# Optimization experiments

Measured on AMD Instinct MI355X. Metric: run time of the kernel, lower is better.

Reference implementation:

```python
import jax, jax.numpy as jnp
import numpy as np

B, L = 64, 200
NQ = 1024          # n_question == output_dim
NPID = 4096
D = 256            # q_embed_dim
H = 512            # hidden_dim
Q = 1024           # output_dim
L2 = 1e-05


def setup_inputs() -> dict:
    key = jax.random.key(0)
    ks = jax.random.split(key, 20)
    q_data = jax.random.randint(ks[0], (B, L), 1, NQ + 1)          # question ids in [1, NQ]
    ans = jax.random.randint(ks[1], (B, L), 0, 2)
    qa_data = q_data + NQ * ans                                     # encoded (q, answer)
    pid_data = jax.random.randint(ks[2], (B, L), 0, NPID + 1)
    matrix = jax.random.uniform(ks[3], (Q, Q), jnp.float32) * 0.05  # p_c_relations
    u = jax.random.uniform(ks[4], (B, L))
    target = jnp.where(u < 0.1, -1.0, jnp.where(u < 0.55, 0.0, 1.0)).astype(jnp.float32)
    s = 0.05
    q_emb = jax.random.normal(ks[5], (NQ + 1, D), jnp.float32) * s
    qa_emb = jax.random.normal(ks[6], (2, D), jnp.float32) * s
    q_emb_diff = jax.random.normal(ks[7], (NQ + 1, D), jnp.float32) * s
    qa_emb_diff = jax.random.normal(ks[8], (2 * NQ + 1, D), jnp.float32) * s
    diff_parm = jax.random.normal(ks[9], (NPID + 1, 1), jnp.float32) * s
    gs = 1.0 / np.sqrt(H).astype(np.float32)
    w_ih = jax.random.uniform(ks[10], (3 * H, 2 * D), jnp.float32, -gs, gs)
    w_hh = jax.random.uniform(ks[11], (3 * H, H), jnp.float32, -gs, gs)
    b_ih = jax.random.uniform(ks[12], (3 * H,), jnp.float32, -gs, gs)
    b_hh = jax.random.uniform(ks[13], (3 * H,), jnp.float32, -gs, gs)
    fc_w = jax.random.normal(ks[14], (Q, H), jnp.float32) * 0.02
    fc_b = jnp.zeros((Q,), jnp.float32)
    return dict(q_data=q_data, qa_data=qa_data, pid_data=pid_data, matrix=matrix,
                target=target, q_emb=q_emb, qa_emb=qa_emb, q_emb_diff=q_emb_diff,
                qa_emb_diff=qa_emb_diff, diff_parm=diff_parm, w_ih=w_ih, w_hh=w_hh,
                b_ih=b_ih, b_hh=b_hh, fc_w=fc_w, fc_b=fc_b)


def _gru(x, w_ih, w_hh, b_ih, b_hh):
    # PyTorch GRU, single layer, batch_first. x: [B, L, In]
    xg = jnp.einsum('bli,gi->blg', x, w_ih) + b_ih          # [B, L, 3H]
    def step(h, xg_t):
        hg = h @ w_hh.T + b_hh
        xr, xz, xn = jnp.split(xg_t, 3, axis=-1)
        hr, hz, hn = jnp.split(hg, 3, axis=-1)
        r = jax.nn.sigmoid(xr + hr)
        z = jax.nn.sigmoid(xz + hz)
        n = jnp.tanh(xn + r * hn)
        h_new = (1.0 - z) * n + z * h
        return h_new, h_new
    h0 = jnp.zeros((x.shape[0], w_hh.shape[1]), x.dtype)
    _, hs = jax.lax.scan(step, h0, xg.transpose(1, 0, 2))
    return hs.transpose(1, 0, 2)                             # [B, L, H]


def reference(q_data, qa_data, pid_data, matrix, target, q_emb, qa_emb,
              q_emb_diff, qa_emb_diff, diff_parm, w_ih, w_hh, b_ih, b_hh,
              fc_w, fc_b):
    q_embed = q_emb[q_data]                                  # [B, L, D]
    qa = (qa_data - q_data) // NQ                            # answer in {0,1}
    qa_embed = qa_emb[qa] + q_embed
    pid_embed = diff_parm[pid_data]                          # [B, L, 1]
    q_embed2 = q_embed + pid_embed * q_emb_diff[q_data]
    qa_embed2 = qa_embed + pid_embed * qa_emb_diff[qa]
    c_reg = (pid_embed ** 2).sum() * L2

    x = jnp.concatenate([qa_embed2, q_embed2], axis=-1)      # [B, L, 2D]
    gru_out = _gru(x, w_ih, w_hh, b_ih, b_hh)
    gru_out = jnp.einsum('blh,qh->blq', gru_out, fc_w) + fc_b  # [B, L, Q]

    got = jnp.einsum('blq,kq->blk', gru_out, matrix)         # [B, L, Q]
    master = jnp.where(got >= 0.4, 1.0, got)                 # threshold-to-1 only
    # mastery of the question asked at step t: master[b, t, q-1]
    mvals = jnp.take_along_axis(master, (q_data - 1)[..., None], axis=2)[..., 0]  # [B, L]

    f32 = jnp.float32
    eq = (q_data[:, :, None] == q_data[:, None, :]).astype(f32)   # [B, t, k]
    t_idx = jnp.arange(L)
    tri_strict = (t_idx[:, None] > t_idx[None, :]).astype(f32)    # k < t
    tri_incl = (t_idx[:, None] >= t_idx[None, :]).astype(f32)     # k <= t
    mast = (mvals == 1.0).astype(f32)
    notm = (mvals == 0.0).astype(f32)
    qa1 = (qa == 1).astype(f32)
    qa0 = 1.0 - qa1
    base = eq * tri_strict                                        # [B, L, L]
    mc = jnp.einsum('btk,bk->bt', base, qa1 * mast)   # master_correct
    mi = jnp.einsum('btk,bk->bt', base, qa0 * mast)   # master_incorrect
    nmc = jnp.einsum('btk,bk->bt', base, qa0 * notm)  # no_master_correct
    aa = jnp.einsum('btk,tk->bt', eq, tri_incl)       # answered_all (>= 1)

    arB = jnp.arange(B)
    idx = q_data - 1

    def dina_step(carry, xs):
        guess, slip = carry                            # [B, Q] each
        i_t, m_t, qa_t, mc_t, mi_t, nmc_t, aa_t = xs   # [B] each
        g_upd = jnp.where(m_t == 1.0, mc_t / aa_t,
                          jnp.where(qa_t == 0, 1.0 - nmc_t / aa_t, nmc_t / aa_t))
        upd_slip = (m_t == 1.0) & (qa_t == 0)
        new_g = jnp.where(upd_slip, guess[arB, i_t], g_upd)
        new_s = jnp.where(upd_slip, mi_t / aa_t, slip[arB, i_t])
        guess = guess.at[arB, i_t].set(new_g)
        slip = slip.at[arB, i_t].set(new_s)
        p = (1.0 - new_s) * (m_t * new_g + (1.0 - new_s) * (1.0 - m_t))
        return (guess, slip), p

    init = (jnp.zeros((B, Q), f32), jnp.zeros((B, Q), f32))
    xs = (idx.T, mvals.T, qa.T, mc.T, mi.T, nmc.T, aa.T)
    _, ps = jax.lax.scan(dina_step, init, xs)          # [L, B]
    preds = ps.T.reshape(-1)                           # [B*L]

    labels = target.reshape(-1)
    mask = labels > -0.9
    preds_d = jax.lax.stop_gradient(preds)             # torch detaches via torch.tensor()
    mse_sum = (((preds_d - labels) ** 2) * mask.astype(f32)).sum()
    loss = mse_sum + c_reg
    return (loss, jax.nn.sigmoid(preds_d), mask.sum())
```

## Files before the change

kernel.cpp:

```cpp
#include <hip/hip_runtime.h>
#include <hip/hip_bf16.h>
#include <math.h>

#define BB 64
#define LL 200
#define NQ 1024
#define DD 256
#define HH 512
#define QQ 1024
#define G3 1536
#define BL 12800
#define GBLK 256

#define OFF_ACC   ((size_t)0)
#define OFF_CELLS ((size_t)16)
#define OFF_HA    ((size_t)1056)
#define OFF_AQ    (OFF_HA + 65536)
#define OFF_DQ    (OFF_AQ + 1574400)
#define OFF_BQA   (OFF_DQ + 1574400)
#define OFF_CQA   (OFF_BQA + 3072)
#define OFF_WSUM  (OFF_CQA + 3072)
#define OFF_FCWT  (OFF_WSUM + 393216)
#define OFF_M2    (OFF_FCWT + 524288)
#define OFF_MB    (OFF_M2 + 524288)
#define OFF_QINT  (OFF_MB + 1024)
#define OFF_QAINT (OFF_QINT + 12800)
#define OFF_PIDF  (OFF_QAINT + 12800)

typedef float f32x4 __attribute__((ext_vector_type(4)));

__device__ __forceinline__ float wave_sum64(float v) {
    #pragma unroll
    for (int o = 32; o > 0; o >>= 1) v += __shfl_down(v, o, 64);
    return v;
}

__device__ __forceinline__ f32x4 llc_load4(const float* p) {
    f32x4 v;
    asm volatile("global_load_dwordx4 %0, %1, off sc0 sc1" : "=v"(v) : "v"(p));
    return v;
}
__device__ __forceinline__ void llc_wait2(f32x4& a, f32x4& b) {
    asm volatile("s_waitcnt vmcnt(0)" : "+v"(a), "+v"(b));
}
__device__ __forceinline__ void llc_store1(float* p, float v) {
    asm volatile("global_store_dword %0, %1, off sc0 sc1" :: "v"(p), "v"(v) : "memory");
}

__device__ __forceinline__ float quad_sum(float v) {
    float t1 = __int_as_float(__builtin_amdgcn_update_dpp(
        0, __float_as_int(v), 0xB1, 0xF, 0xF, true));
    v += t1;
    float t2 = __int_as_float(__builtin_amdgcn_update_dpp(
        0, __float_as_int(v), 0x4E, 0xF, 0xF, true));
    return v + t2;
}

__device__ __forceinline__ void gemm_nt_body(
    const float* __restrict__ A, int lda, const float* __restrict__ B, int ldb,
    float* __restrict__ C, int ldc, int M, int N, int K,
    const float* __restrict__ bias, int bm, int bn, int tid, bool sumB,
    float (*As)[129], float (*Bs)[65])
{
    const int tx = tid & 15, ty = tid >> 4;
    const int mm = tid >> 4, kk = tid & 15;
    float acc[8][4] = {};
    float ar[8], br[4];
    #pragma unroll
    for (int i = 0; i < 8; ++i) {
        int m = bm + mm + 16 * i;
        ar[i] = (m < M) ? A[(size_t)m * lda + kk] : 0.f;
    }
    #pragma unroll
    for (int i = 0; i < 4; ++i) {
        int n = bn + mm + 16 * i;
        br[i] = (n < N) ? (sumB ? (B[(size_t)n * ldb + kk] + B[(size_t)n * ldb + DD + kk])
                                : B[(size_t)n * ldb + kk]) : 0.f;
    }
    for (int k0 = 0; k0 < K; k0 += 16) {
        #pragma unroll
        for (int i = 0; i < 8; ++i) As[kk][mm + 16 * i] = ar[i];
        #pragma unroll
        for (int i = 0; i < 4; ++i) Bs[kk][mm + 16 * i] = br[i];
        __syncthreads();
        int kn = k0 + 16;
        if (kn < K) {
            #pragma unroll
            for (int i = 0; i < 8; ++i) {
                int m = bm + mm + 16 * i;
                ar[i] = (m < M) ? A[(size_t)m * lda + kn + kk] : 0.f;
            }
            #pragma unroll
            for (int i = 0; i < 4; ++i) {
                int n = bn + mm + 16 * i;
                br[i] = (n < N) ? (sumB ? (B[(size_t)n * ldb + kn + kk]
                                           + B[(size_t)n * ldb + DD + kn + kk])
                                        : B[(size_t)n * ldb + kn + kk]) : 0.f;
            }
        }
        #pragma unroll
        for (int kq = 0; kq < 16; ++kq) {
            float a[8], b[4];
            #pragma unroll
            for (int i = 0; i < 8; ++i) a[i] = As[kq][ty * 8 + i];
            #pragma unroll
            for (int j = 0; j < 4; ++j) b[j] = Bs[kq][tx * 4 + j];
            #pragma unroll
            for (int i = 0; i < 8; ++i)
                #pragma unroll
                for (int j = 0; j < 4; ++j) acc[i][j] += a[i] * b[j];
        }
        __syncthreads();
    }
    #pragma unroll
    for (int i = 0; i < 8; ++i) {
        int m = bm + ty * 8 + i;
        if (m >= M) continue;
        #pragma unroll
        for (int j = 0; j < 4; ++j) {
            int n = bn + tx * 4 + j;
            if (n >= N) continue;
            C[(size_t)m * ldc + n] = acc[i][j] + (bias ? bias[n] : 0.f);
        }
    }
}

__global__ __launch_bounds__(256) void prep_all(
    const float* __restrict__ q_emb, const float* __restrict__ q_emb_diff,
    const float* __restrict__ qa_emb, const float* __restrict__ qa_emb_diff,
    const float* __restrict__ w_ih, const float* __restrict__ b_ih,
    float* __restrict__ Aq, float* __restrict__ Dq,
    float* __restrict__ Bqa, float* __restrict__ Cqa,
    const float* __restrict__ matrix, const float* __restrict__ fc_w,
    const float* __restrict__ fc_b, float* __restrict__ M2, float* __restrict__ mb,
    const int* __restrict__ q_data, const int* __restrict__ qa_data,
    const int* __restrict__ pid_data, const float* __restrict__ diff_parm,
    int* __restrict__ qint, int* __restrict__ qaint, float* __restrict__ pidf,
    float* __restrict__ acc_g, float* __restrict__ hA)
{
    __shared__ float As[16][129];
    __shared__ float Bs[16][65];
    __shared__ float sm[4];
    const int tid = threadIdx.x;
    const int widx = blockIdx.x;

    if (widx < 128) {
        const int bm = (widx >> 3) * 64, bn = (widx & 7) * 64;
        const int kk = tid & 15, mm = tid >> 4;
        const int nb = tid & 63, kb2 = tid >> 6;
        const int tx = tid & 15, ty = tid >> 4;
        float acc[4][4] = {};
        for (int k0 = 0; k0 < QQ; k0 += 16) {
            if (k0) __syncthreads();
            #pragma unroll
            for (int i = 0; i < 4; ++i)
                As[kk][mm + 16 * i] = matrix[(size_t)(bm + mm + 16 * i) * QQ + k0 + kk];
            #pragma unroll
            for (int i = 0; i < 4; ++i)
                Bs[kb2 + 4 * i][nb] = fc_w[(size_t)(k0 + kb2 + 4 * i) * HH + bn + nb];
            __syncthreads();
            #pragma unroll
            for (int kq = 0; kq < 16; ++kq) {
                float a[4], b[4];
                #pragma unroll
                for (int i = 0; i < 4; ++i) a[i] = As[kq][ty * 4 + i];
                #pragma unroll
                for (int j = 0; j < 4; ++j) b[j] = Bs[kq][tx * 4 + j];
                #pragma unroll
                for (int i = 0; i < 4; ++i)
                    #pragma unroll
                    for (int j = 0; j < 4; ++j) acc[i][j] += a[i] * b[j];
            }
        }
        #pragma unroll
        for (int i = 0; i < 4; ++i)
            #pragma unroll
            for (int j = 0; j < 4; ++j)
                M2[(size_t)(bm + ty * 4 + i) * HH + bn + tx * 4 + j] = acc[i][j];
        return;
    }
    if (widx < 560) {
        const int w2 = widx - 128;
        const int z = w2 >= 216;
        const int w3 = z ? w2 - 216 : w2;
        const int bm = (w3 / 24) * 128, bn = (w3 % 24) * 64;
        gemm_nt_body(z ? q_emb_diff : q_emb, DD,
                     z ? (w_ih + DD) : w_ih, 2 * DD,
                     z ? Dq : Aq, G3, NQ + 1, G3, DD,
                     nullptr, bm, bn, tid, !z, As, Bs);
        return;
    }
    if (widx < 608) {
        const int w2 = widx - 560;
        const int z = w2 >= 24;
        const int bn = (z ? w2 - 24 : w2) * 64;
        gemm_nt_body(z ? qa_emb_diff : qa_emb, DD,
                     w_ih, 2 * DD,
                     z ? Cqa : Bqa, G3, 2, G3, DD,
                     z ? nullptr : b_ih, 0, bn, tid, false, As, Bs);
        return;
    }
    if (widx < 612) {
        const int wv2 = tid >> 6, lane2 = tid & 63;
        const int kb = (widx - 608) * 256 + wv2 * 64;
        for (int i = 0; i < 64; ++i) {
            const float* mrow = matrix + (size_t)(kb + i) * QQ;
            float sacc = 0.f;
            #pragma unroll
            for (int j = 0; j < 16; ++j)
                sacc += mrow[lane2 + 64 * j] * fc_b[lane2 + 64 * j];
            sacc = wave_sum64(sacc);
            if (lane2 == 0) mb[kb + i] = sacc;
        }
        return;
    }
    if (widx < 662) {
        int r = (widx - 612) * 256 + tid;
        float pp = 0.f;
        if (r < BL) {
            int q = q_data[r];
            qint[r] = q;
            qaint[r] = (qa_data[r] - q) / NQ;
            float pid = diff_parm[pid_data[r]];
            pidf[r] = pid;
            pp = pid * pid;
        }
        pp = wave_sum64(pp);
        int lane = tid & 63, w = tid >> 6;
        if (lane == 0) sm[w] = pp;
        __syncthreads();
        if (tid == 0) atomicAdd(&acc_g[0], sm[0] + sm[1] + sm[2] + sm[3]);
        return;
    }
    {
        float* dst = hA + (size_t)(widx - 662) * 4096 + tid;
        #pragma unroll
        for (int i = 0; i < 16; ++i) dst[i * 256] = 0.f;
    }
}

__global__ __launch_bounds__(512) void gru_persist(
    const float* __restrict__ Aq,
    const float* __restrict__ Dq,
    const float* __restrict__ Bqa,
    const float* __restrict__ Cqa,
    const int* __restrict__ qint,
    const int* __restrict__ qaint,
    const float* __restrict__ pidf,
    const float* __restrict__ w_hh,
    const float* __restrict__ b_hh,
    float* __restrict__ hA,
    const float* __restrict__ M2,
    const float* __restrict__ mbv,
    unsigned int* __restrict__ cells,
    const float* __restrict__ target,
    float* __restrict__ out,
    float* __restrict__ acc_g)
{
    __shared__ float hs[8][512];
    __shared__ float part[8][3][16][8];
    __shared__ float bqs[2][3][16];
    __shared__ float cqs[2][3][16];
    __shared__ int smq[8][200];
    __shared__ int smqa[8][200];
    __shared__ float smp[8][200];
    __shared__ float mvbuf[LL];

    const int tid = threadIdx.x;
    const int bid = blockIdx.x;
    const int bg = bid >> 5;
    const int ug = bid & 31;
    const int j0 = ug * 16;
    const int wv = tid >> 6;
    const int lane = tid & 63;
    const int g = lane >> 2;
    const int s = lane & 3;

    if (tid < 96) {
        const int qa = tid / 48, rem = tid - qa * 48;
        const int gate = rem >> 4, u = rem & 15;
        bqs[qa][gate][u] = Bqa[(size_t)qa * G3 + gate * HH + j0 + u];
        cqs[qa][gate][u] = Cqa[(size_t)qa * G3 + gate * HH + j0 + u];
    }
    for (int i = tid; i < 8 * LL; i += 512) {
        const int c = i / LL, tt = i - c * LL;
        const int col = bg * 8 + c;
        smq[c][tt] = qint[col * LL + tt];
        smqa[c][tt] = qaint[col * LL + tt];
        smp[c][tt] = pidf[col * LL + tt];
    }

    f32x4 ws4[3][4];
    #pragma unroll
    for (int gate = 0; gate < 3; ++gate)
        #pragma unroll
        for (int q = 0; q < 4; ++q)
            ws4[gate][q] = *(const f32x4*)&w_hh[
                (size_t)(gate * HH + j0 + g) * HH + wv * 64 + q * 16 + s * 4];

    const int eu = tid >> 3;
    const int eb = tid & 7;
    float bhr = 0.f, bhz = 0.f, bhn = 0.f;
    if (tid < 128) {
        bhr = b_hh[j0 + eu];
        bhz = b_hh[HH + j0 + eu];
        bhn = b_hh[2 * HH + j0 + eu];
    }

    const int b0 = lane >> 4;
    const int c0 = (lane & 15) * 4;

    __syncthreads();

    for (int t = 0; t < LL; ++t) {
        float xr = 0.f, xz = 0.f, xn = 0.f;
        if (tid < 128) {
            const int q = smq[eb][t];
            const int qa = smqa[eb][t];
            const float pid = smp[eb][t];
            const float* aq = Aq + (size_t)q * G3 + j0 + eu;
            const float* dq = Dq + (size_t)q * G3 + j0 + eu;
            float ar_ = aq[0], az_ = aq[HH], an_ = aq[2 * HH];
            float dr_ = dq[0], dz_ = dq[HH], dn_ = dq[2 * HH];
            xr = ar_ + bqs[qa][0][eu] + pid * (cqs[qa][0][eu] + dr_);
            xz = az_ + bqs[qa][1][eu] + pid * (cqs[qa][1][eu] + dz_);
            xn = an_ + bqs[qa][2][eu] + pid * (cqs[qa][2][eu] + dn_);
        }
        f32x4 m2a = {0.f, 0.f, 0.f, 0.f}, m2b = {0.f, 0.f, 0.f, 0.f};
        float mbq = 0.f;
        if (wv == 2 && ug < 8 && t >= 1) {
            const int q = smq[ug][t - 1] - 1;
            const float* m2r = M2 + (size_t)q * HH + lane * 8;
            m2a = *(const f32x4*)m2r;
            m2b = *(const f32x4*)(m2r + 4);
            mbq = mbv[q];
        }
        if (t && tid < 64) {
            const unsigned want = (unsigned)t;
            for (;;) {
                unsigned v = want;
                if (lane < 32)
                    v = __hip_atomic_load(&cells[(bg * 32 + lane) * 4],
                                          __ATOMIC_RELAXED, __HIP_MEMORY_SCOPE_AGENT);
                if (__all((int)(v >= want))) break;
                __builtin_amdgcn_s_sleep(2);
            }
        }
        __syncthreads();

        {
            const float* hcur = hA + (size_t)(t & 1) * (HH * BB);
            const float* p0 = hcur + (size_t)(bg * 8 + b0) * HH + wv * 64 + c0;
            f32x4 va = llc_load4(p0);
            f32x4 vb = llc_load4(p0 + 4 * HH);
            llc_wait2(va, vb);
            *(f32x4*)&hs[wv][b0 * 64 + ((c0 + 8 * b0) & 63)] = va;
            *(f32x4*)&hs[wv][(b0 + 4) * 64 + ((c0 + 8 * b0 + 32) & 63)] = vb;
        }

        float acc[3][8];
        #pragma unroll
        for (int gate = 0; gate < 3; ++gate) {
            #pragma unroll
            for (int b = 0; b < 8; ++b) acc[gate][b] = 0.f;
        }
        #pragma unroll
        for (int q = 0; q < 4; ++q) {
            const int cb = q * 16 + s * 4;
            #pragma unroll
            for (int b = 0; b < 8; ++b) {
                f32x4 h4 = *(const f32x4*)&hs[wv][b * 64 + ((cb + 8 * b) & 63)];
                #pragma unroll
                for (int gate = 0; gate < 3; ++gate) {
                    acc[gate][b] += ws4[gate][q].x * h4.x + ws4[gate][q].y * h4.y
                                  + ws4[gate][q].z * h4.z + ws4[gate][q].w * h4.w;
                }
            }
        }

        #pragma unroll
        for (int gate = 0; gate < 3; ++gate)
            #pragma unroll
            for (int b = 0; b < 8; ++b)
                acc[gate][b] = quad_sum(acc[gate][b]);

        if (s < 3) {
            const int rot = (2 * ((g >> 2) + s)) & 7;
            #pragma unroll
            for (int hp = 0; hp < 4; ++hp) {
                const int b = hp * 2;
                float e0 = (s == 0) ? acc[0][b]     : (s == 1) ? acc[1][b]     : acc[2][b];
                float e1 = (s == 0) ? acc[0][b + 1] : (s == 1) ? acc[1][b + 1] : acc[2][b + 1];
                const int bp = (b + rot) & 7;
                *(float2*)&part[wv][s][g][bp] = make_float2(e0, e1);
            }
        }
        __syncthreads();

        if (wv == 2 && ug < 8 && t >= 1) {
            float sacc = 0.f;
            #pragma unroll
            for (int j = 0; j < 8; ++j) {
                const int k = lane * 8 + j;
                const float hv = hs[k >> 6][ug * 64 + (((k & 63) + 8 * ug) & 63)];
                const float mvw = (j == 0) ? m2a.x : (j == 1) ? m2a.y : (j == 2) ? m2a.z
                                : (j == 3) ? m2a.w : (j == 4) ? m2b.x : (j == 5) ? m2b.y
                                : (j == 6) ? m2b.z : m2b.w;
                sacc += hv * mvw;
            }
            sacc = wave_sum64(sacc);
            if (lane == 0) {
                float sv = sacc + mbq;
                mvbuf[t - 1] = (sv >= 0.4f) ? 1.0f : sv;
            }
        }

        if (tid < 128) {
            const int rb = eu >> 2;
            const int bp0 = (eb + 2 * (rb + 0)) & 7;
            const int bp1 = (eb + 2 * (rb + 1)) & 7;
            const int bp2 = (eb + 2 * (rb + 2)) & 7;
            float sg0 = 0.f, sg1 = 0.f, sg2 = 0.f;
            #pragma unroll
            for (int w = 0; w < 8; ++w) {
                sg0 += part[w][0][eu][bp0];
                sg1 += part[w][1][eu][bp1];
                sg2 += part[w][2][eu][bp2];
            }
            const int ku = j0 + eu;
            float hprev = hs[ku >> 6][eb * 64 + (((ku & 63) + 8 * eb) & 63)];
            float rg = 1.f / (1.f + expf(-(xr + sg0 + bhr)));
            float zg = 1.f / (1.f + expf(-(xz + sg1 + bhz)));
            float ng = tanhf(xn + rg * (sg2 + bhn));
            float hn = (1.f - zg) * ng + zg * hprev;
            llc_store1(hA + (size_t)((t + 1) & 1) * (HH * BB)
                          + (size_t)(bg * 8 + eb) * HH + ku, hn);
            asm volatile("s_waitcnt vmcnt(0)" ::: "memory");
        }
        __syncthreads();
        if (tid == 0)
            __hip_atomic_store(&cells[bid * 4], (unsigned)(t + 1),
                               __ATOMIC_RELAXED, __HIP_MEMORY_SCOPE_AGENT);
    }

    if (ug >= 8) return;
    if (tid < 64) {
        const unsigned want = (unsigned)LL;
        for (;;) {
            unsigned v = want;
            if (lane < 32)
                v = __hip_atomic_load(&cells[(bg * 32 + lane) * 4],
                                      __ATOMIC_RELAXED, __HIP_MEMORY_SCOPE_AGENT);
            if (__all((int)(v >= want))) break;
            __builtin_amdgcn_s_sleep(2);
        }
    }
    __syncthreads();
    {
        const float* hcur = hA + (size_t)(LL & 1) * (HH * BB);
        const float* p0 = hcur + (size_t)(bg * 8 + b0) * HH + wv * 64 + c0;
        f32x4 va = llc_load4(p0);
        f32x4 vb = llc_load4(p0 + 4 * HH);
        llc_wait2(va, vb);
        *(f32x4*)&hs[wv][b0 * 64 + ((c0 + 8 * b0) & 63)] = va;
        *(f32x4*)&hs[wv][(b0 + 4) * 64 + ((c0 + 8 * b0 + 32) & 63)] = vb;
    }
    __syncthreads();
    if (wv == 2) {
        const int q = smq[ug][LL - 1] - 1;
        const float* m2r = M2 + (size_t)q * HH + lane * 8;
        f32x4 ma = *(const f32x4*)m2r;
        f32x4 mc4 = *(const f32x4*)(m2r + 4);
        float sacc = 0.f;
        #pragma unroll
        for (int j = 0; j < 8; ++j) {
            const int k = lane * 8 + j;
            const float hv = hs[k >> 6][ug * 64 + (((k & 63) + 8 * ug) & 63)];
            const float mvw = (j == 0) ? ma.x : (j == 1) ? ma.y : (j == 2) ? ma.z
                            : (j == 3) ? ma.w : (j == 4) ? mc4.x : (j == 5) ? mc4.y
                            : (j == 6) ? mc4.z : mc4.w;
            sacc += hv * mvw;
        }
        sacc = wave_sum64(sacc);
        if (lane == 0) {
            float sv = sacc + mbv[q];
            mvbuf[LL - 1] = (sv >= 0.4f) ? 1.0f : sv;
        }
    }
    __syncthreads();

    const int bq = bg * 8 + ug;
    float* guess = &hs[0][0];
    float* slip = &hs[2][0];
    float* preds_l = &hs[4][0];
    float* s_mc = &part[0][0][0][0];
    float* s_mi = s_mc + 256;
    float* s_nmc = s_mc + 512;
    float* s_aa = s_mc + 768;
    float* sred = &bqs[0][0][0];
    float* cred = sred + 8;
    for (int i = tid; i < QQ; i += 512) { guess[i] = 0.f; slip[i] = 0.f; }
    if (tid < LL) {
        const int qt = smq[ug][tid];
        float smc = 0.f, smi = 0.f, snmc = 0.f, saa = 0.f;
        for (int k = 0; k <= tid; ++k) {
            if (smq[ug][k] == qt) {
                saa += 1.f;
                if (k < tid) {
                    float mk = (mvbuf[k] == 1.f) ? 1.f : 0.f;
                    float nk = (mvbuf[k] == 0.f) ? 1.f : 0.f;
                    float a1 = (smqa[ug][k] == 1) ? 1.f : 0.f;
                    smc += a1 * mk;
                    smi += (1.f - a1) * mk;
                    snmc += (1.f - a1) * nk;
                }
            }
        }
        s_mc[tid] = smc;
        s_mi[tid] = smi;
        s_nmc[tid] = snmc;
        s_aa[tid] = saa;
    }
    __syncthreads();
    if (tid == 0) {
        for (int t = 0; t < LL; ++t) {
            const int i = smq[ug][t] - 1;
            const float m = mvbuf[t];
            const int qa = smqa[ug][t];
            const float aat = s_aa[t];
            float g_upd = (m == 1.f) ? s_mc[t] / aat
                          : ((qa == 0) ? 1.f - s_nmc[t] / aat : s_nmc[t] / aat);
            bool us = (m == 1.f) && (qa == 0);
            float ng = us ? guess[i] : g_upd;
            float ns = us ? s_mi[t] / aat : slip[i];
            guess[i] = ng;
            slip[i] = ns;
            preds_l[t] = (1.f - ns) * (m * ng + (1.f - ns) * (1.f - m));
        }
    }
    __syncthreads();
    if (tid < 256) {
        float lm = 0.f, lc = 0.f;
        if (tid < LL) {
            const float p = preds_l[tid];
            const float lab = target[bq * LL + tid];
            const float msk = (lab > -0.9f) ? 1.f : 0.f;
            const float d = p - lab;
            lm = d * d * msk;
            lc = msk;
            out[1 + bq * LL + tid] = 1.f / (1.f + expf(-p));
        }
        lm = wave_sum64(lm);
        lc = wave_sum64(lc);
        if (lane == 0) { sred[wv] = lm; cred[wv] = lc; }
    }
    __syncthreads();
    if (tid == 0) {
        atomicAdd(&acc_g[1], sred[0] + sred[1] + sred[2] + sred[3]);
        atomicAdd(&acc_g[2], cred[0] + cred[1] + cred[2] + cred[3]);
        const unsigned old = __hip_atomic_fetch_add(&cells[1021], 1u,
                                                    __ATOMIC_ACQ_REL,
                                                    __HIP_MEMORY_SCOPE_AGENT);
        if (old == 63) {
            float a0 = __hip_atomic_load(&acc_g[0], __ATOMIC_RELAXED, __HIP_MEMORY_SCOPE_AGENT);
            float a1 = __hip_atomic_load(&acc_g[1], __ATOMIC_RELAXED, __HIP_MEMORY_SCOPE_AGENT);
            float a2 = __hip_atomic_load(&acc_g[2], __ATOMIC_RELAXED, __HIP_MEMORY_SCOPE_AGENT);
            out[0] = a1 + a0 * 1e-5f;
            out[1 + BL] = a2;
        }
    }
}

extern "C" void kernel_launch(void* const* d_in, const int* in_sizes, int n_in,
                              void* d_out, int out_size, void* d_ws, size_t ws_size,
                              hipStream_t stream) {
    const int* q_data = (const int*)d_in[0];
    const int* qa_data = (const int*)d_in[1];
    const int* pid_data = (const int*)d_in[2];
    const float* matrix = (const float*)d_in[3];
    const float* target = (const float*)d_in[4];
    const float* q_emb = (const float*)d_in[5];
    const float* qa_emb = (const float*)d_in[6];
    const float* q_emb_diff = (const float*)d_in[7];
    const float* qa_emb_diff = (const float*)d_in[8];
    const float* diff_parm = (const float*)d_in[9];
    const float* w_ih = (const float*)d_in[10];
    const float* w_hh = (const float*)d_in[11];
    const float* b_ih = (const float*)d_in[12];
    const float* b_hh = (const float*)d_in[13];
    const float* fc_w = (const float*)d_in[14];
    const float* fc_b = (const float*)d_in[15];
    float* out = (float*)d_out;
    float* W = (float*)d_ws;

    float* acc = W + OFF_ACC;
    unsigned int* cells = (unsigned int*)(W + OFF_CELLS);
    float* hA = W + OFF_HA;
    float* Aq = W + OFF_AQ;
    float* Dq = W + OFF_DQ;
    float* Bqa = W + OFF_BQA;
    float* Cqa = W + OFF_CQA;
    float* M2 = W + OFF_M2;
    float* mb = W + OFF_MB;
    int* qint = (int*)(W + OFF_QINT);
    int* qaint = (int*)(W + OFF_QAINT);
    float* pidf = W + OFF_PIDF;

    hipMemsetAsync(W, 0, 1056 * sizeof(float), stream);

    prep_all<<<678, 256, 0, stream>>>(
        q_emb, q_emb_diff, qa_emb, qa_emb_diff, w_ih, b_ih,
        Aq, Dq, Bqa, Cqa, matrix, fc_w, fc_b, M2, mb,
        q_data, qa_data, pid_data, diff_parm, qint, qaint, pidf, acc, hA);

    gru_persist<<<GBLK, 512, 0, stream>>>(Aq, Dq, Bqa, Cqa, qint, qaint, pidf,
                                          w_hh, b_hh, hA, M2, mb, cells,
                                          target, out, acc);
}
```

Measured before the change: 1.005 ms.

## Parallelize DINA scan per timestep, fold memset into prep, drop per-step barrier

The serial single-thread DINA recurrence over 200 steps is replaced by per-timestep threads that scan backwards for the last guess/slip update of the same question, turning a sequential loop into parallel lookback. The hipMemsetAsync of the counter/accumulator region is folded into an extra prep_all block, and the pid-regularizer atomics become per-block partial stores summed at the end. In the GRU step loop every thread now spins on the cell flags itself and the following __syncthreads is removed, which cuts a barrier but raises polling traffic and risks hs buffer reuse hazards.

```diff
diff --git a/kernel.cpp b/kernel.cpp
--- a/kernel.cpp
+++ b/kernel.cpp
@@ -19,8 +19,8 @@
 #define OFF_DQ    (OFF_AQ + 1574400)
 #define OFF_BQA   (OFF_DQ + 1574400)
 #define OFF_CQA   (OFF_BQA + 3072)
-#define OFF_WSUM  (OFF_CQA + 3072)
-#define OFF_FCWT  (OFF_WSUM + 393216)
+#define OFF_CREGS (OFF_CQA + 3072)
+#define OFF_FCWT  (OFF_CREGS + 393216)
 #define OFF_M2    (OFF_FCWT + 524288)
 #define OFF_MB    (OFF_M2 + 524288)
 #define OFF_QINT  (OFF_MB + 1024)
@@ -136,7 +136,7 @@
     const int* __restrict__ q_data, const int* __restrict__ qa_data,
     const int* __restrict__ pid_data, const float* __restrict__ diff_parm,
     int* __restrict__ qint, int* __restrict__ qaint, float* __restrict__ pidf,
-    float* __restrict__ acc_g, float* __restrict__ hA)
+    float* __restrict__ cregs, float* __restrict__ hA, float* __restrict__ Wbase)
 {
     __shared__ float As[16][129];
     __shared__ float Bs[16][65];
@@ -229,14 +229,16 @@
         int lane = tid & 63, w = tid >> 6;
         if (lane == 0) sm[w] = pp;
         __syncthreads();
-        if (tid == 0) atomicAdd(&acc_g[0], sm[0] + sm[1] + sm[2] + sm[3]);
+        if (tid == 0) cregs[widx - 612] = sm[0] + sm[1] + sm[2] + sm[3];
         return;
     }
-    {
+    if (widx < 678) {
         float* dst = hA + (size_t)(widx - 662) * 4096 + tid;
         #pragma unroll
         for (int i = 0; i < 16; ++i) dst[i * 256] = 0.f;
-    }
+        return;
+    }
+    for (int i = tid; i < 1056; i += 256) Wbase[i] = 0.f;
 }
 
 __global__ __launch_bounds__(512) void gru_persist(
@@ -255,7 +257,8 @@
     unsigned int* __restrict__ cells,
     const float* __restrict__ target,
     float* __restrict__ out,
-    float* __restrict__ acc_g)
+    float* __restrict__ acc_g,
+    const float* __restrict__ cregs)
 {
     __shared__ float hs[8][512];
     __shared__ float part[8][3][16][8];
@@ -335,7 +338,7 @@
             m2b = *(const f32x4*)(m2r + 4);
             mbq = mbv[q];
         }
-        if (t && tid < 64) {
+        if (t) {
             const unsigned want = (unsigned)t;
             for (;;) {
                 unsigned v = want;
@@ -346,7 +349,6 @@
                 __builtin_amdgcn_s_sleep(2);
             }
         }
-        __syncthreads();
 
         {
             const float* hcur = hA + (size_t)(t & 1) * (HH * BB);
@@ -490,8 +492,6 @@
     __syncthreads();
 
     const int bq = bg * 8 + ug;
-    float* guess = &hs[0][0];
-    float* slip = &hs[2][0];
     float* preds_l = &hs[4][0];
     float* s_mc = &part[0][0][0][0];
     float* s_mi = s_mc + 256;
@@ -499,7 +499,6 @@
     float* s_aa = s_mc + 768;
     float* sred = &bqs[0][0][0];
     float* cred = sred + 8;
-    for (int i = tid; i < QQ; i += 512) { guess[i] = 0.f; slip[i] = 0.f; }
     if (tid < LL) {
         const int qt = smq[ug][tid];
         float smc = 0.f, smi = 0.f, snmc = 0.f, saa = 0.f;
@@ -522,21 +521,35 @@
         s_aa[tid] = saa;
     }
     __syncthreads();
-    if (tid == 0) {
-        for (int t = 0; t < LL; ++t) {
-            const int i = smq[ug][t] - 1;
-            const float m = mvbuf[t];
-            const int qa = smqa[ug][t];
-            const float aat = s_aa[t];
-            float g_upd = (m == 1.f) ? s_mc[t] / aat
-                          : ((qa == 0) ? 1.f - s_nmc[t] / aat : s_nmc[t] / aat);
-            bool us = (m == 1.f) && (qa == 0);
-            float ng = us ? guess[i] : g_upd;
-            float ns = us ? s_mi[t] / aat : slip[i];
-            guess[i] = ng;
-            slip[i] = ns;
-            preds_l[t] = (1.f - ns) * (m * ng + (1.f - ns) * (1.f - m));
-        }
+    if (tid < LL) {
+        const int t = tid;
+        const int qt = smq[ug][t];
+        const float m = mvbuf[t];
+        const int qa = smqa[ug][t];
+        const bool ust = (m == 1.f) && (qa == 0);
+        float gval = 0.f, sval = 0.f;
+        bool gf = false, sf = false;
+        for (int k = t - 1; k >= 0; --k) {
+            if (gf && sf) break;
+            if (smq[ug][k] != qt) continue;
+            const float mk = mvbuf[k];
+            const int qak = smqa[ug][k];
+            const bool usk = (mk == 1.f) && (qak == 0);
+            if (usk) {
+                if (!sf) { sval = s_mi[k] / s_aa[k]; sf = true; }
+            } else {
+                if (!gf) {
+                    gval = (mk == 1.f) ? s_mc[k] / s_aa[k]
+                         : ((qak == 0) ? 1.f - s_nmc[k] / s_aa[k] : s_nmc[k] / s_aa[k]);
+                    gf = true;
+                }
+            }
+        }
+        const float g_upd = (m == 1.f) ? s_mc[t] / s_aa[t]
+                          : ((qa == 0) ? 1.f - s_nmc[t] / s_aa[t] : s_nmc[t] / s_aa[t]);
+        const float ng = ust ? gval : g_upd;
+        const float ns = ust ? s_mi[t] / s_aa[t] : sval;
+        preds_l[t] = (1.f - ns) * (m * ng + (1.f - ns) * (1.f - m));
     }
     __syncthreads();
     if (tid < 256) {
@@ -562,10 +575,11 @@
                                                     __ATOMIC_ACQ_REL,
                                                     __HIP_MEMORY_SCOPE_AGENT);
         if (old == 63) {
-            float a0 = __hip_atomic_load(&acc_g[0], __ATOMIC_RELAXED, __HIP_MEMORY_SCOPE_AGENT);
+            float cr = 0.f;
+            for (int i = 0; i < 50; ++i) cr += cregs[i];
             float a1 = __hip_atomic_load(&acc_g[1], __ATOMIC_RELAXED, __HIP_MEMORY_SCOPE_AGENT);
             float a2 = __hip_atomic_load(&acc_g[2], __ATOMIC_RELAXED, __HIP_MEMORY_SCOPE_AGENT);
-            out[0] = a1 + a0 * 1e-5f;
+            out[0] = a1 + cr * 1e-5f;
             out[1 + BL] = a2;
         }
     }
@@ -600,20 +614,19 @@
     float* Dq = W + OFF_DQ;
     float* Bqa = W + OFF_BQA;
     float* Cqa = W + OFF_CQA;
+    float* cregs = W + OFF_CREGS;
     float* M2 = W + OFF_M2;
     float* mb = W + OFF_MB;
     int* qint = (int*)(W + OFF_QINT);
     int* qaint = (int*)(W + OFF_QAINT);
     float* pidf = W + OFF_PIDF;
 
-    hipMemsetAsync(W, 0, 1056 * sizeof(float), stream);
-
-    prep_all<<<678, 256, 0, stream>>>(
+    prep_all<<<679, 256, 0, stream>>>(
         q_emb, q_emb_diff, qa_emb, qa_emb_diff, w_ih, b_ih,
         Aq, Dq, Bqa, Cqa, matrix, fc_w, fc_b, M2, mb,
-        q_data, qa_data, pid_data, diff_parm, qint, qaint, pidf, acc, hA);
+        q_data, qa_data, pid_data, diff_parm, qint, qaint, pidf, cregs, hA, W);
 
     gru_persist<<<GBLK, 512, 0, stream>>>(Aq, Dq, Bqa, Cqa, qint, qaint, pidf,
                                           w_hh, b_hh, hA, M2, mb, cells,
-                                          target, out, acc);
-}
+                                          target, out, acc, cregs);
+}
```

After: 1.136 ms. 13.1% more time.
